# Performance work log

Measured on AMD Instinct MI355X. Metric: run time of the kernel, lower is better.

Reference implementation:

```python
import jax, jax.numpy as jnp
import numpy as np
import math

T, E = 8192, 64            # tokens, experts
K_VALUE = 2                # top-2 router
CAP_FACTOR = 1.25          # capacity_factor_train (module in training mode)
MIN_CAPACITY = 4


def _get_capacity(tokens, experts):
    cap = math.floor(K_VALUE * CAP_FACTOR * tokens / experts)
    cap += cap % 2  # make even
    cap = max(cap, MIN_CAPACITY)
    assert cap > 0
    return int(cap)


def setup_inputs() -> dict:
    key = jax.random.key(0)
    inputs = jax.random.normal(key, (T, E), dtype=jnp.float32)
    return {"inputs": inputs}


def reference(inputs):
    tokens, experts = inputs.shape
    capacity = _get_capacity(tokens, experts)  # static (shape-derived)

    probs = jax.nn.softmax(inputs, axis=-1)                       # [T, E]
    top1_idx = jnp.argmax(probs, axis=-1)                         # [T]
    mask1 = jax.nn.one_hot(top1_idx, experts, dtype=jnp.int32)    # [T, E]
    probs_except1 = jnp.where(mask1.astype(bool), -jnp.inf, probs)
    top2_idx = jnp.argmax(probs_except1, axis=-1)                 # [T]
    mask2 = jax.nn.one_hot(top2_idx, experts, dtype=jnp.int32)

    # position of each token in its expert's queue (moe_cumsum = cumsum - 1)
    rank1 = jnp.cumsum(mask1, axis=0) - 1                          # [T, E]
    rank2 = jnp.cumsum(mask2, axis=0) - 1 + jnp.sum(mask1, axis=0, keepdims=True)

    # drop tokens beyond capacity
    mask1 = mask1 * (rank1 < capacity)
    mask2 = mask2 * (rank2 < capacity)
    used_capacity = mask1.sum(axis=0) + mask2.sum(axis=0)          # [E]

    # per-token slot index (0 if dropped) and gate weight (0 if dropped)
    r1 = jnp.sum(mask1 * rank1, axis=-1)                           # [T]
    r2 = jnp.sum(mask2 * rank2, axis=-1)
    w1 = jnp.sum(mask1 * probs, axis=-1)                           # [T]
    w2 = jnp.sum(mask2 * probs, axis=-1)
    m1b = jnp.sum(mask1, axis=-1).astype(bool)                     # kept flags
    m2b = jnp.sum(mask2, axis=-1).astype(bool)

    idx = jnp.arange(tokens)
    cb_weight = jnp.zeros((tokens, experts, capacity), dtype=inputs.dtype)
    cb_weight = cb_weight.at[idx, top1_idx, r1].add(w1)
    cb_weight = cb_weight.at[idx, top2_idx, r2].add(w2)

    sec_mask = jnp.zeros((tokens, experts, capacity), dtype=bool)
    sec_mask = sec_mask.at[idx, top1_idx, r1].max(m1b)
    sec_mask = sec_mask.at[idx, top2_idx, r2].max(m2b)

    return used_capacity, cb_weight, sec_mask
```

## Files before the change

### kernel.cpp

```cpp
#include <hip/hip_runtime.h>
#include <hip/hip_bf16.h>
#include <math.h>

#define T_TOKENS 8192
#define N_EXP    64
#define CAP      320
#define ROW4     (N_EXP * CAP / 4)

typedef float f32x4 __attribute__((ext_vector_type(4)));

__global__ __launch_bounds__(256) void moe_topk_kernel(
    const float* __restrict__ in,
    int* __restrict__ top1, int* __restrict__ top2,
    float* __restrict__ w1, float* __restrict__ w2)
{
    const int token = blockIdx.x * 4 + (threadIdx.x >> 6);
    const int lane  = threadIdx.x & 63;
    if (token >= T_TOKENS) return;

    const float x = in[(size_t)token * N_EXP + lane];

    float v = x; int idx = lane;
    #pragma unroll
    for (int off = 32; off; off >>= 1) {
        float vo = __shfl_xor(v, off);
        int   io = __shfl_xor(idx, off);
        if (vo > v || (vo == v && io < idx)) { v = vo; idx = io; }
    }
    const float m  = v;
    const int   i1 = idx;

    float s = expf(x - m);
    #pragma unroll
    for (int off = 32; off; off >>= 1) s += __shfl_xor(s, off);

    float v2 = (lane == i1) ? -INFINITY : x;
    int idx2 = lane;
    #pragma unroll
    for (int off = 32; off; off >>= 1) {
        float vo = __shfl_xor(v2, off);
        int   io = __shfl_xor(idx2, off);
        if (vo > v2 || (vo == v2 && io < idx2)) { v2 = vo; idx2 = io; }
    }

    if (lane == 0) {
        top1[token] = i1;
        top2[token] = idx2;
        w1[token]   = 1.0f / s;
        w2[token]   = expf(v2 - m) / s;
    }
}

__global__ __launch_bounds__(1024) void moe_rank_kernel(
    const int* __restrict__ top1, const int* __restrict__ top2,
    int* __restrict__ c1, int* __restrict__ c2,
    float* __restrict__ used)
{
    const int e    = blockIdx.x;
    const int tid  = threadIdx.x;
    const int lane = tid & 63;
    const int wid  = tid >> 6;

    __shared__ int wsA[16], wsB[16];

    const int4 a1 = ((const int4*)top1)[tid * 2];
    const int4 b1 = ((const int4*)top1)[tid * 2 + 1];
    const int m0 = (a1.x == e), m1 = (a1.y == e), m2 = (a1.z == e), m3 = (a1.w == e);
    const int m4 = (b1.x == e), m5 = (b1.y == e), m6 = (b1.z == e), m7 = (b1.w == e);
    const int cnt1 = m0 + m1 + m2 + m3 + m4 + m5 + m6 + m7;

    int sc = cnt1;
    #pragma unroll
    for (int off = 1; off < 64; off <<= 1) {
        int n = __shfl_up(sc, off);
        if (lane >= off) sc += n;
    }
    if (lane == 63) wsA[wid] = sc;
    __syncthreads();
    int wbase = 0, total1 = 0;
    #pragma unroll
    for (int w = 0; w < 16; ++w) {
        const int sv = wsA[w];
        if (w < wid) wbase += sv;
        total1 += sv;
    }
    {
        int r = wbase + sc - cnt1;
        const int t0 = tid * 8;
        if (m0) { c1[t0 + 0] = (r < CAP) ? (e * CAP + r) : -1; ++r; }
        if (m1) { c1[t0 + 1] = (r < CAP) ? (e * CAP + r) : -1; ++r; }
        if (m2) { c1[t0 + 2] = (r < CAP) ? (e * CAP + r) : -1; ++r; }
        if (m3) { c1[t0 + 3] = (r < CAP) ? (e * CAP + r) : -1; ++r; }
        if (m4) { c1[t0 + 4] = (r < CAP) ? (e * CAP + r) : -1; ++r; }
        if (m5) { c1[t0 + 5] = (r < CAP) ? (e * CAP + r) : -1; ++r; }
        if (m6) { c1[t0 + 6] = (r < CAP) ? (e * CAP + r) : -1; ++r; }
        if (m7) { c1[t0 + 7] = (r < CAP) ? (e * CAP + r) : -1; ++r; }
    }

    const int4 a2 = ((const int4*)top2)[tid * 2];
    const int4 b2 = ((const int4*)top2)[tid * 2 + 1];
    const int n0 = (a2.x == e), n1 = (a2.y == e), n2 = (a2.z == e), n3 = (a2.w == e);
    const int n4 = (b2.x == e), n5 = (b2.y == e), n6 = (b2.z == e), n7 = (b2.w == e);
    const int cnt2 = n0 + n1 + n2 + n3 + n4 + n5 + n6 + n7;

    int sc2 = cnt2;
    #pragma unroll
    for (int off = 1; off < 64; off <<= 1) {
        int n = __shfl_up(sc2, off);
        if (lane >= off) sc2 += n;
    }
    if (lane == 63) wsB[wid] = sc2;
    __syncthreads();
    int wbase2 = 0, total2 = 0;
    #pragma unroll
    for (int w = 0; w < 16; ++w) {
        const int sv = wsB[w];
        if (w < wid) wbase2 += sv;
        total2 += sv;
    }
    {
        int r = total1 + wbase2 + sc2 - cnt2;
        const int t0 = tid * 8;
        if (n0) { c2[t0 + 0] = (r < CAP) ? (e * CAP + r) : -1; ++r; }
        if (n1) { c2[t0 + 1] = (r < CAP) ? (e * CAP + r) : -1; ++r; }
        if (n2) { c2[t0 + 2] = (r < CAP) ? (e * CAP + r) : -1; ++r; }
        if (n3) { c2[t0 + 3] = (r < CAP) ? (e * CAP + r) : -1; ++r; }
        if (n4) { c2[t0 + 4] = (r < CAP) ? (e * CAP + r) : -1; ++r; }
        if (n5) { c2[t0 + 5] = (r < CAP) ? (e * CAP + r) : -1; ++r; }
        if (n6) { c2[t0 + 6] = (r < CAP) ? (e * CAP + r) : -1; ++r; }
        if (n7) { c2[t0 + 7] = (r < CAP) ? (e * CAP + r) : -1; ++r; }
    }

    if (tid == 0) {
        const int kept1 = min(total1, CAP);
        const int kept2 = min(max(CAP - total1, 0), total2);
        used[e] = (float)(kept1 + kept2);
    }
}

__global__ __launch_bounds__(256) void moe_row_write_kernel(
    const int* __restrict__ c1, const int* __restrict__ c2,
    const float* __restrict__ w1, const float* __restrict__ w2,
    float* __restrict__ out)
{
    const int b   = blockIdx.x;
    const int tid = threadIdx.x;
    const bool is_sec = (b >= T_TOKENS);
    const int t   = is_sec ? (b - T_TOKENS) : b;

    const int   p1 = c1[t];
    const int   p2 = c2[t];
    const float a  = is_sec ? 1.0f : w1[t];
    const float c  = is_sec ? 1.0f : w2[t];
    const int   q1 = p1 >> 2;
    const int   q2 = p2 >> 2;

    f32x4* __restrict__ row = (f32x4*)(out + N_EXP) + (size_t)b * ROW4;

    #pragma unroll
    for (int i = 0; i < ROW4 / 256; ++i) {
        const int idx = i * 256 + tid;
        f32x4 v = {0.f, 0.f, 0.f, 0.f};
        if (idx == q1 || idx == q2) {
            const int base = idx * 4;
            #pragma unroll
            for (int j = 0; j < 4; ++j) {
                const int pos = base + j;
                float vv = 0.f;
                if (pos == p1) vv += a;
                if (pos == p2) vv += c;
                v[j] = vv;
            }
        }
        row[idx] = v;
    }
}

extern "C" void kernel_launch(void* const* d_in, const int* in_sizes, int n_in,
                              void* d_out, int out_size, void* d_ws, size_t ws_size,
                              hipStream_t stream) {
    const float* in  = (const float*)d_in[0];
    float*       out = (float*)d_out;

    int*   top1 = (int*)d_ws;
    int*   top2 = top1 + T_TOKENS;
    int*   c1   = top2 + T_TOKENS;
    int*   c2   = c1 + T_TOKENS;
    float* w1   = (float*)(c2 + T_TOKENS);
    float* w2   = w1 + T_TOKENS;

    moe_topk_kernel<<<T_TOKENS / 4, 256, 0, stream>>>(in, top1, top2, w1, w2);
    moe_rank_kernel<<<N_EXP, 1024, 0, stream>>>(top1, top2, c1, c2, out);
    moe_row_write_kernel<<<2 * T_TOKENS, 256, 0, stream>>>(c1, c2, w1, w2, out);
}
```

Before: 259.6 us.

## Replace dense row-write kernel with memset plus sparse scatter in rank kernel

Drops the kernel that wrote every element of both the dispatch-weight and mask tensors and instead zero-fills the whole output with hipMemsetAsync. The rank kernel now scatters the kept gate weights and mask ones straight to their final positions. This also removes the intermediate slot-index buffers and one launch. The cost is still a full-output write, now done by the runtime memset path, followed by uncoalesced scattered stores that depend on the memset finishing first.

```diff
diff --git a/kernel.cpp b/kernel.cpp
--- a/kernel.cpp
+++ b/kernel.cpp
@@ -5,9 +5,7 @@
 #define T_TOKENS 8192
 #define N_EXP    64
 #define CAP      320
-#define ROW4     (N_EXP * CAP / 4)
-
-typedef float f32x4 __attribute__((ext_vector_type(4)));
+#define ROWSZ    (N_EXP * CAP)
 
 __global__ __launch_bounds__(256) void moe_topk_kernel(
     const float* __restrict__ in,
@@ -51,10 +49,10 @@
     }
 }
 
-__global__ __launch_bounds__(1024) void moe_rank_kernel(
+__global__ __launch_bounds__(1024) void moe_rank_scatter_kernel(
     const int* __restrict__ top1, const int* __restrict__ top2,
-    int* __restrict__ c1, int* __restrict__ c2,
-    float* __restrict__ used)
+    const float* __restrict__ w1, const float* __restrict__ w2,
+    float* __restrict__ out)
 {
     const int e    = blockIdx.x;
     const int tid  = threadIdx.x;
@@ -62,6 +60,9 @@
     const int wid  = tid >> 6;
 
     __shared__ int wsA[16], wsB[16];
+
+    float* __restrict__ cb  = out + N_EXP;
+    float* __restrict__ sec = cb + (size_t)T_TOKENS * ROWSZ;
 
     const int4 a1 = ((const int4*)top1)[tid * 2];
     const int4 b1 = ((const int4*)top1)[tid * 2 + 1];
@@ -87,14 +88,18 @@
     {
         int r = wbase + sc - cnt1;
         const int t0 = tid * 8;
-        if (m0) { c1[t0 + 0] = (r < CAP) ? (e * CAP + r) : -1; ++r; }
-        if (m1) { c1[t0 + 1] = (r < CAP) ? (e * CAP + r) : -1; ++r; }
-        if (m2) { c1[t0 + 2] = (r < CAP) ? (e * CAP + r) : -1; ++r; }
-        if (m3) { c1[t0 + 3] = (r < CAP) ? (e * CAP + r) : -1; ++r; }
-        if (m4) { c1[t0 + 4] = (r < CAP) ? (e * CAP + r) : -1; ++r; }
-        if (m5) { c1[t0 + 5] = (r < CAP) ? (e * CAP + r) : -1; ++r; }
-        if (m6) { c1[t0 + 6] = (r < CAP) ? (e * CAP + r) : -1; ++r; }
-        if (m7) { c1[t0 + 7] = (r < CAP) ? (e * CAP + r) : -1; ++r; }
+        #define SCAT1(K, MK)                                                  \
+            if (MK) {                                                         \
+                if (r < CAP) {                                                \
+                    const size_t o = (size_t)(t0 + K) * ROWSZ + e * CAP + r;  \
+                    cb[o]  = w1[t0 + K];                                      \
+                    sec[o] = 1.0f;                                            \
+                }                                                             \
+                ++r;                                                          \
+            }
+        SCAT1(0, m0) SCAT1(1, m1) SCAT1(2, m2) SCAT1(3, m3)
+        SCAT1(4, m4) SCAT1(5, m5) SCAT1(6, m6) SCAT1(7, m7)
+        #undef SCAT1
     }
 
     const int4 a2 = ((const int4*)top2)[tid * 2];
@@ -121,58 +126,24 @@
     {
         int r = total1 + wbase2 + sc2 - cnt2;
         const int t0 = tid * 8;
-        if (n0) { c2[t0 + 0] = (r < CAP) ? (e * CAP + r) : -1; ++r; }
-        if (n1) { c2[t0 + 1] = (r < CAP) ? (e * CAP + r) : -1; ++r; }
-        if (n2) { c2[t0 + 2] = (r < CAP) ? (e * CAP + r) : -1; ++r; }
-        if (n3) { c2[t0 + 3] = (r < CAP) ? (e * CAP + r) : -1; ++r; }
-        if (n4) { c2[t0 + 4] = (r < CAP) ? (e * CAP + r) : -1; ++r; }
-        if (n5) { c2[t0 + 5] = (r < CAP) ? (e * CAP + r) : -1; ++r; }
-        if (n6) { c2[t0 + 6] = (r < CAP) ? (e * CAP + r) : -1; ++r; }
-        if (n7) { c2[t0 + 7] = (r < CAP) ? (e * CAP + r) : -1; ++r; }
+        #define SCAT2(K, NK)                                                  \
+            if (NK) {                                                         \
+                if (r < CAP) {                                                \
+                    const size_t o = (size_t)(t0 + K) * ROWSZ + e * CAP + r;  \
+                    cb[o]  = w2[t0 + K];                                      \
+                    sec[o] = 1.0f;                                            \
+                }                                                             \
+                ++r;                                                          \
+            }
+        SCAT2(0, n0) SCAT2(1, n1) SCAT2(2, n2) SCAT2(3, n3)
+        SCAT2(4, n4) SCAT2(5, n5) SCAT2(6, n6) SCAT2(7, n7)
+        #undef SCAT2
     }
 
     if (tid == 0) {
         const int kept1 = min(total1, CAP);
         const int kept2 = min(max(CAP - total1, 0), total2);
-        used[e] = (float)(kept1 + kept2);
-    }
-}
-
-__global__ __launch_bounds__(256) void moe_row_write_kernel(
-    const int* __restrict__ c1, const int* __restrict__ c2,
-    const float* __restrict__ w1, const float* __restrict__ w2,
-    float* __restrict__ out)
-{
-    const int b   = blockIdx.x;
-    const int tid = threadIdx.x;
-    const bool is_sec = (b >= T_TOKENS);
-    const int t   = is_sec ? (b - T_TOKENS) : b;
-
-    const int   p1 = c1[t];
-    const int   p2 = c2[t];
-    const float a  = is_sec ? 1.0f : w1[t];
-    const float c  = is_sec ? 1.0f : w2[t];
-    const int   q1 = p1 >> 2;
-    const int   q2 = p2 >> 2;
-
-    f32x4* __restrict__ row = (f32x4*)(out + N_EXP) + (size_t)b * ROW4;
-
-    #pragma unroll
-    for (int i = 0; i < ROW4 / 256; ++i) {
-        const int idx = i * 256 + tid;
-        f32x4 v = {0.f, 0.f, 0.f, 0.f};
-        if (idx == q1 || idx == q2) {
-            const int base = idx * 4;
-            #pragma unroll
-            for (int j = 0; j < 4; ++j) {
-                const int pos = base + j;
-                float vv = 0.f;
-                if (pos == p1) vv += a;
-                if (pos == p2) vv += c;
-                v[j] = vv;
-            }
-        }
-        row[idx] = v;
+        out[e] = (float)(kept1 + kept2);
     }
 }
 
@@ -184,12 +155,11 @@
 
     int*   top1 = (int*)d_ws;
     int*   top2 = top1 + T_TOKENS;
-    int*   c1   = top2 + T_TOKENS;
-    int*   c2   = c1 + T_TOKENS;
-    float* w1   = (float*)(c2 + T_TOKENS);
+    float* w1   = (float*)(top2 + T_TOKENS);
     float* w2   = w1 + T_TOKENS;
 
+    hipMemsetAsync(d_out, 0, (size_t)out_size * sizeof(float), stream);
+
     moe_topk_kernel<<<T_TOKENS / 4, 256, 0, stream>>>(in, top1, top2, w1, w2);
-    moe_rank_kernel<<<N_EXP, 1024, 0, stream>>>(top1, top2, c1, c2, out);
-    moe_row_write_kernel<<<2 * T_TOKENS, 256, 0, stream>>>(c1, c2, w1, w2, out);
+    moe_rank_scatter_kernel<<<N_EXP, 1024, 0, stream>>>(top1, top2, w1, w2, out);
 }
```

New measurement: 232.4 us. 10.5% less time.
